# Kernel optimization log

Measured on AMD Instinct MI355X. Metric: run time of the kernel, lower is better.

Reference implementation:

```python
import jax, jax.numpy as jnp
import numpy as np

HEADS = 16
HEAD_DIM = 1024 // HEADS  # 64
SCALE = float(np.sqrt(HEAD_DIM))  # math.sqrt(features // heads)


def setup_inputs() -> dict:
    key = jax.random.key(0)
    ks = jax.random.split(key, 6)
    n, m, d, c = 2048, 2048, 1024, 768
    return {
        "x": jax.random.normal(ks[0], (n, d), dtype=jnp.float32),
        "ctx": jax.random.normal(ks[1], (m, c), dtype=jnp.float32),
        "Wq": jax.random.normal(ks[2], (d, d), dtype=jnp.float32) * (1.0 / np.sqrt(d)),
        "Wk": jax.random.normal(ks[3], (c, d), dtype=jnp.float32) * (1.0 / np.sqrt(c)),
        "Wv": jax.random.normal(ks[4], (c, d), dtype=jnp.float32) * (1.0 / np.sqrt(c)),
        "Wo": jax.random.normal(ks[5], (d, d), dtype=jnp.float32) * (1.0 / np.sqrt(d)),
    }


def reference(x, ctx, Wq, Wk, Wv, Wo):
    n, d = x.shape
    q = (x @ Wq).reshape(n, HEADS, HEAD_DIM).transpose(1, 0, 2)      # h n d
    k = (ctx @ Wk).reshape(-1, HEADS, HEAD_DIM).transpose(1, 0, 2)   # h m d
    v = (ctx @ Wv).reshape(-1, HEADS, HEAD_DIM).transpose(1, 0, 2)   # h m d
    scores = jnp.einsum("hnd,hmd->hnm", q, k) / SCALE
    attn = jax.nn.softmax(scores, axis=-1)
    out = jnp.einsum("hnm,hmd->hnd", attn, v)                        # h n d
    out = out.transpose(1, 0, 2).reshape(n, d)                       # n (h d)
    return out @ Wo
```

## Files before the change

kernel.cpp:

```cpp
#include <hip/hip_runtime.h>
#include <hip/hip_bf16.h>
#include <stdint.h>

typedef unsigned short bfu;
typedef __attribute__((ext_vector_type(8))) short short8;
typedef __attribute__((ext_vector_type(4))) float f32x4;

#define LOG2E 1.4426950408889634f

__device__ __forceinline__ bfu f2bf(float f) {
  union { float f; uint32_t u; } v; v.f = f;
  uint32_t r = (v.u + 0x7fffu + ((v.u >> 16) & 1u)) >> 16;
  return (bfu)r;
}

__device__ __forceinline__ void gload16(const void* g, void* l) {
  __builtin_amdgcn_global_load_lds((const __attribute__((address_space(1))) void*)g,
                                   (__attribute__((address_space(3))) void*)l, 16, 0, 0);
}

__device__ __forceinline__ void conv_body(const float* __restrict__ in, bfu* __restrict__ out,
                                          int i) {
  const float4* p = (const float4*)in + (size_t)i * 2;
  float4 a = p[0], b = p[1];
  union { bfu h[8]; uint4 v; } o;
  o.h[0] = f2bf(a.x); o.h[1] = f2bf(a.y); o.h[2] = f2bf(a.z); o.h[3] = f2bf(a.w);
  o.h[4] = f2bf(b.x); o.h[5] = f2bf(b.y); o.h[6] = f2bf(b.z); o.h[7] = f2bf(b.w);
  ((uint4*)out)[i] = o.v;
}

__device__ __forceinline__ void trans_body(const float* __restrict__ W, bfu* __restrict__ WT,
                                           int Kd, int n0, int k0) {
  __shared__ float tile[32][33];
  const int tx = threadIdx.x & 31, ty = threadIdx.x >> 5;
#pragma unroll
  for (int i = 0; i < 32; i += 8)
    tile[ty + i][tx] = W[(size_t)(k0 + ty + i) * 1024 + n0 + tx];
  __syncthreads();
#pragma unroll
  for (int i = 0; i < 32; i += 8)
    WT[(size_t)(n0 + ty + i) * Kd + k0 + tx] = f2bf(tile[tx][ty + i]);
}

__global__ __launch_bounds__(256) void prep_kernel(
    const float* __restrict__ x, const float* __restrict__ ctx,
    const float* __restrict__ Wq, const float* __restrict__ Wk,
    const float* __restrict__ Wv, const float* __restrict__ Wo,
    bfu* xb, bfu* ctxb, bfu* WTq, bfu* WTk, bfu* WTv, bfu* WTo) {
  int b = blockIdx.x;
  if (b < 1024)       conv_body(x, xb, b * 256 + threadIdx.x);
  else if (b < 1792)  conv_body(ctx, ctxb, (b - 1024) * 256 + threadIdx.x);
  else if (b < 2816) { b -= 1792; trans_body(Wq, WTq, 1024, (b & 31) * 32, (b >> 5) * 32); }
  else if (b < 3584) { b -= 2816; trans_body(Wk, WTk, 768, (b & 31) * 32, (b >> 5) * 32); }
  else if (b < 4352) { b -= 3584; trans_body(Wv, WTv, 768, (b & 31) * 32, (b >> 5) * 32); }
  else               { b -= 4352; trans_body(Wo, WTo, 1024, (b & 31) * 32, (b >> 5) * 32); }
}

typedef bfu Tile128[2][4][128][8];

__device__ __forceinline__ void gemm128_body(Tile128& As2, Tile128& Bs2,
    const bfu* __restrict__ A, const bfu* __restrict__ BT,
    bfu* __restrict__ Cb, int N, int K, float scale, int m0, int n0) {
  const int tid = threadIdx.x, lane = tid & 63, wave = tid >> 6;
  const int g = lane >> 4, c = lane & 15;
  const int wm = (wave >> 1) * 64, wn = (wave & 1) * 64;
  const int nt = K / 32;

  auto stage = [&](int buf, int kt) {
#pragma unroll
    for (int u = 0; u < 4; ++u) {
      int idx = wave * 4 + u;
      if (idx < 8) {
        int kg = idx & 3, rb = idx >> 2;
        gload16(&A[(size_t)(m0 + rb * 64 + lane) * K + kt + kg * 8], &As2[buf][kg][rb * 64][0]);
      } else {
        int kg = (idx - 8) & 3, rb = (idx - 8) >> 2;
        gload16(&BT[(size_t)(n0 + rb * 64 + lane) * K + kt + kg * 8], &Bs2[buf][kg][rb * 64][0]);
      }
    }
  };

  f32x4 acc[4][4] = {};
  stage(0, 0);
  for (int t = 0; t < nt; ++t) {
    __syncthreads();
    if (t + 1 < nt) stage((t + 1) & 1, (t + 1) * 32);
    const int b = t & 1;
    short8 af[4], bfr[4];
#pragma unroll
    for (int i = 0; i < 4; ++i) {
      af[i]  = *(const short8*)&As2[b][g][wm + i * 16 + c][0];
      bfr[i] = *(const short8*)&Bs2[b][g][wn + i * 16 + c][0];
    }
#pragma unroll
    for (int i = 0; i < 4; ++i)
#pragma unroll
      for (int j = 0; j < 4; ++j)
        acc[i][j] = __builtin_amdgcn_mfma_f32_16x16x32_bf16(af[i], bfr[j], acc[i][j], 0, 0, 0);
  }
#pragma unroll
  for (int i = 0; i < 4; ++i)
#pragma unroll
    for (int j = 0; j < 4; ++j) {
      int row = m0 + wm + i * 16 + g * 4;
      int col = n0 + wn + j * 16 + c;
#pragma unroll
      for (int r = 0; r < 4; ++r)
        Cb[(size_t)(row + r) * N + col] = f2bf(acc[i][j][r] * scale);
    }
}

typedef bfu AsArr[2][4][128][8];
typedef bfu BsArr[2][4][64][8];

__device__ __forceinline__ void gemm_body(AsArr& As2, BsArr& Bs2,
    const bfu* __restrict__ A, const bfu* __restrict__ BT,
    bfu* __restrict__ Cb, float* __restrict__ Cf,
    int N, int K, float scale, int m0, int n0) {
  const int tid = threadIdx.x, lane = tid & 63, wave = tid >> 6;
  const int g = lane >> 4, c = lane & 15;
  const int wm = wave * 32;
  const int nt = K / 32;

  auto stage = [&](int buf, int kt) {
#pragma unroll
    for (int u = 0; u < 3; ++u) {
      int idx = wave * 3 + u;
      if (idx < 8) {
        int g2 = idx & 3, rb = idx >> 2;
        gload16(&A[(size_t)(m0 + rb * 64 + lane) * K + kt + g2 * 8], &As2[buf][g2][rb * 64][0]);
      } else {
        int g2 = idx - 8;
        gload16(&BT[(size_t)(n0 + lane) * K + kt + g2 * 8], &Bs2[buf][g2][0][0]);
      }
    }
  };

  f32x4 acc[2][4] = {};
  stage(0, 0);
  for (int t = 0; t < nt; ++t) {
    __syncthreads();
    if (t + 1 < nt) stage((t + 1) & 1, (t + 1) * 32);
    const int b = t & 1;
    short8 af[2], bfr[4];
#pragma unroll
    for (int i = 0; i < 2; ++i) af[i] = *(const short8*)&As2[b][g][wm + i * 16 + c][0];
#pragma unroll
    for (int j = 0; j < 4; ++j) bfr[j] = *(const short8*)&Bs2[b][g][j * 16 + c][0];
#pragma unroll
    for (int i = 0; i < 2; ++i)
#pragma unroll
      for (int j = 0; j < 4; ++j)
        acc[i][j] = __builtin_amdgcn_mfma_f32_16x16x32_bf16(af[i], bfr[j], acc[i][j], 0, 0, 0);
  }
#pragma unroll
  for (int i = 0; i < 2; ++i)
#pragma unroll
    for (int j = 0; j < 4; ++j) {
      int row = m0 + wm + i * 16 + g * 4;
      int col = n0 + j * 16 + c;
#pragma unroll
      for (int r = 0; r < 4; ++r) {
        float v = acc[i][j][r] * scale;
        if (Cb) Cb[(size_t)(row + r) * N + col] = f2bf(v);
        else    Cf[(size_t)(row + r) * N + col] = v;
      }
    }
}

__global__ __launch_bounds__(256) void gemm3_kernel(
    const bfu* __restrict__ xb, const bfu* __restrict__ WTq, bfu* __restrict__ Qb,
    const bfu* __restrict__ ctxb, const bfu* __restrict__ WTk, bfu* __restrict__ Kb,
    const bfu* __restrict__ WTv, bfu* __restrict__ Vtb) {
  __shared__ alignas(16) bfu As2[2][4][128][8];
  __shared__ alignas(16) bfu Bs2[2][4][128][8];
  int bid = blockIdx.x;
  if (bid < 128)
    gemm128_body(As2, Bs2, xb, WTq, Qb, 1024, 1024, 0.125f * LOG2E, (bid >> 3) * 128, (bid & 7) * 128);
  else if (bid < 256) {
    int r = bid - 128;
    gemm128_body(As2, Bs2, ctxb, WTk, Kb, 1024, 768, 1.0f, (r >> 3) * 128, (r & 7) * 128);
  } else {
    int r = bid - 256;
    gemm_body(*(AsArr*)As2, *(BsArr*)Bs2, WTv, ctxb, Vtb, nullptr,
              2048, 768, 1.0f, (r >> 5) * 128, (r & 31) * 64);
  }
}

__global__ __launch_bounds__(256) void gemmo_kernel(const bfu* __restrict__ AO,
                                                    const bfu* __restrict__ WTo,
                                                    float* __restrict__ out) {
  __shared__ alignas(16) bfu As2[2][4][128][8];
  __shared__ alignas(16) bfu Bs2[2][4][64][8];
  int bid = blockIdx.x;
  gemm_body(As2, Bs2, AO, WTo, nullptr, out, 1024, 1024, 1.0f, (bid >> 4) * 128, (bid & 15) * 64);
}

__global__ __launch_bounds__(256) void attn_kernel(
    const bfu* __restrict__ Q, const bfu* __restrict__ Kmat,
    const bfu* __restrict__ Vt, bfu* __restrict__ O) {
  __shared__ alignas(16) bfu Ks[3][8][64][8];
  __shared__ alignas(16) bfu Vs[3][8][64][8];
  __shared__ alignas(16) bfu Ps[2][64][72];
  const int tid = threadIdx.x, wave = tid >> 6, lane = tid & 63;
  const int g = lane >> 4, c = lane & 15;
  const int bid = blockIdx.x;
  const int xcd = bid & 7, slot = bid >> 3;
  const int h = xcd + 8 * (slot >> 5);
  const int qblk = (slot & 31) * 64;
  const int col0 = h * 64;

  short8 qf[4][2];
#pragma unroll
  for (int qt = 0; qt < 4; ++qt) {
    qf[qt][0] = *(const short8*)&Q[(size_t)(qblk + qt * 16 + c) * 1024 + col0 + g * 8];
    qf[qt][1] = *(const short8*)&Q[(size_t)(qblk + qt * 16 + c) * 1024 + col0 + 32 + g * 8];
  }

  short8 ones;
#pragma unroll
  for (int e = 0; e < 8; ++e) ones[e] = (short)0x3F80;

  f32x4 o_acc[4] = {};
  f32x4 lacc = {};

  auto stage = [&](int buf, int kv0) {
#pragma unroll
    for (int u = 0; u < 4; ++u) {
      int idx = wave * 4 + u;
      if (idx < 8)
        gload16(&Kmat[(size_t)(kv0 + lane) * 1024 + col0 + idx * 8], &Ks[buf][idx][0][0]);
      else
        gload16(&Vt[(size_t)(col0 + lane) * 2048 + kv0 + (idx - 8) * 8], &Vs[buf][idx - 8][0][0]);
    }
  };

  auto qk_exp = [&](int bQ, int pb) {
    short8 kf0 = *(const short8*)&Ks[bQ][g][wave * 16 + c][0];
    short8 kf1 = *(const short8*)&Ks[bQ][4 + g][wave * 16 + c][0];
    f32x4 s[4] = {};
    __builtin_amdgcn_s_setprio(1);
#pragma unroll
    for (int qt = 0; qt < 4; ++qt) {
      s[qt] = __builtin_amdgcn_mfma_f32_16x16x32_bf16(qf[qt][0], kf0, s[qt], 0, 0, 0);
      s[qt] = __builtin_amdgcn_mfma_f32_16x16x32_bf16(qf[qt][1], kf1, s[qt], 0, 0, 0);
    }
    __builtin_amdgcn_s_setprio(0);
#pragma unroll
    for (int qt = 0; qt < 4; ++qt)
#pragma unroll
      for (int j = 0; j < 4; ++j)
        Ps[pb][qt * 16 + g * 4 + j][wave * 16 + c] =
            f2bf(__builtin_amdgcn_exp2f(s[qt][j]));
  };

  auto pv = [&](int pb, int vb) {
    __builtin_amdgcn_s_setprio(1);
#pragma unroll
    for (int kc = 0; kc < 2; ++kc) {
      short8 pf = *(const short8*)&Ps[pb][wave * 16 + c][kc * 32 + g * 8];
      lacc = __builtin_amdgcn_mfma_f32_16x16x32_bf16(pf, ones, lacc, 0, 0, 0);
#pragma unroll
      for (int fd = 0; fd < 4; ++fd) {
        short8 vf = *(const short8*)&Vs[vb][kc * 4 + g][fd * 16 + c][0];
        o_acc[fd] = __builtin_amdgcn_mfma_f32_16x16x32_bf16(pf, vf, o_acc[fd], 0, 0, 0);
      }
    }
    __builtin_amdgcn_s_setprio(0);
  };

  stage(0, 0);
  __syncthreads();
  stage(1, 64);
  qk_exp(0, 0);
  __syncthreads();
  for (int t = 1; t < 32; ++t) {
    stage((t + 1) % 3, ((t + 1) & 31) * 64);
    qk_exp(t % 3, t & 1);
    pv((t - 1) & 1, (t - 1) % 3);
    __syncthreads();
  }
  pv(1, 1);

  const int q0 = qblk + wave * 16;
#pragma unroll
  for (int fd = 0; fd < 4; ++fd)
#pragma unroll
    for (int j = 0; j < 4; ++j) {
      float v = o_acc[fd][j] / lacc[j];
      O[(size_t)(q0 + g * 4 + j) * 1024 + col0 + fd * 16 + c] = f2bf(v);
    }
}

extern "C" void kernel_launch(void* const* d_in, const int* in_sizes, int n_in,
                              void* d_out, int out_size, void* d_ws, size_t ws_size,
                              hipStream_t stream) {
  const float* x   = (const float*)d_in[0];
  const float* ctx = (const float*)d_in[1];
  const float* Wq  = (const float*)d_in[2];
  const float* Wk  = (const float*)d_in[3];
  const float* Wv  = (const float*)d_in[4];
  const float* Wo  = (const float*)d_in[5];
  float* out = (float*)d_out;

  bfu* ws   = (bfu*)d_ws;
  bfu* xb   = ws;
  bfu* WTk  = xb + 2048 * 1024;
  bfu* WTv  = WTk + 1024 * 768;
  bfu* WTo  = WTv + 1024 * 768;
  bfu* Qb   = WTo + 1024 * 1024;
  bfu* Kb   = Qb + 2048 * 1024;
  bfu* Vtb  = Kb + 2048 * 1024;
  bfu* WTq  = (bfu*)d_out;
  bfu* ctxb = WTq + 1024 * 1024;

  dim3 blk(256);
  prep_kernel<<<5376, blk, 0, stream>>>(x, ctx, Wq, Wk, Wv, Wo, xb, ctxb, WTq, WTk, WTv, WTo);
  gemm3_kernel<<<512, blk, 0, stream>>>(xb, WTq, Qb, ctxb, WTk, Kb, WTv, Vtb);
  attn_kernel<<<512, blk, 0, stream>>>(Qb, Kb, Vtb, xb);
  gemmo_kernel<<<256, blk, 0, stream>>>(xb, WTo, out);
}
```

Before: 106.8 us.

## Rewrite output projection GEMM with 64x64 tiles, 128-thread blocks, XCD-aware mapping

The output projection GEMM gets a dedicated kernel that uses 64x64 output tiles and 128-thread blocks, launching 512 blocks instead of 256. Each block's tile is chosen from an XCD-aware mapping of the block id. The goal is more blocks to fill the GPU's compute units, and better L2 locality on the 2048x1024 by 1024x1024 GEMM. The cost is less reuse per block, a different K-tile schedule, and scalar stores of the fp32 output that may coalesce poorly.

```diff
diff --git a/kernel.cpp b/kernel.cpp
--- a/kernel.cpp
+++ b/kernel.cpp
@@ -187,13 +187,60 @@
   }
 }
 
-__global__ __launch_bounds__(256) void gemmo_kernel(const bfu* __restrict__ AO,
+typedef bfu T64[2][4][64][8];
+
+__global__ __launch_bounds__(128) void gemmo_kernel(const bfu* __restrict__ AO,
                                                     const bfu* __restrict__ WTo,
                                                     float* __restrict__ out) {
-  __shared__ alignas(16) bfu As2[2][4][128][8];
+  __shared__ alignas(16) bfu As2[2][4][64][8];
   __shared__ alignas(16) bfu Bs2[2][4][64][8];
-  int bid = blockIdx.x;
-  gemm_body(As2, Bs2, AO, WTo, nullptr, out, 1024, 1024, 1.0f, (bid >> 4) * 128, (bid & 15) * 64);
+  const int tid = threadIdx.x, lane = tid & 63, wave = tid >> 6;
+  const int g = lane >> 4, c = lane & 15;
+  const int bid = blockIdx.x;
+  const int xcd = bid & 7, slot = bid >> 3;
+  const int m0 = (xcd * 4 + (slot >> 4)) * 64;
+  const int n0 = (slot & 15) * 64;
+  const int wm = wave * 32;
+  const int K = 1024, N = 1024, nt = 32;
+
+  auto stage = [&](int buf, int kt) {
+#pragma unroll
+    for (int u = 0; u < 4; ++u) {
+      int idx = wave * 4 + u;
+      if (idx < 4)
+        gload16(&AO[(size_t)(m0 + lane) * K + kt + idx * 8], &As2[buf][idx][lane][0]);
+      else
+        gload16(&WTo[(size_t)(n0 + lane) * K + kt + (idx - 4) * 8], &Bs2[buf][idx - 4][lane][0]);
+    }
+  };
+
+  f32x4 acc[2][4] = {};
+  stage(0, 0);
+  for (int t = 0; t < nt; ++t) {
+    __syncthreads();
+    if (t + 1 < nt) stage((t + 1) & 1, (t + 1) * 32);
+    const int b = t & 1;
+    short8 af[2], bfr[4];
+#pragma unroll
+    for (int i = 0; i < 2; ++i) af[i] = *(const short8*)&As2[b][g][wm + i * 16 + c][0];
+#pragma unroll
+    for (int j = 0; j < 4; ++j) bfr[j] = *(const short8*)&Bs2[b][g][j * 16 + c][0];
+#pragma unroll
+    for (int i = 0; i < 2; ++i)
+#pragma unroll
+      for (int j = 0; j < 4; ++j)
+        acc[i][j] = __builtin_amdgcn_mfma_f32_16x16x32_bf16(af[i], bfr[j], acc[i][j], 0, 0, 0);
+  }
+#pragma unroll
+  for (int i = 0; i < 2; ++i)
+#pragma unroll
+    for (int j = 0; j < 4; ++j) {
+      int row = m0 + wm + i * 16 + g * 4;
+      int col = n0 + j * 16 + c;
+#pragma unroll
+      for (int r = 0; r < 4; ++r)
+        out[(size_t)(row + r) * N + col] = acc[i][j][r];
+    }
 }
 
 __global__ __launch_bounds__(256) void attn_kernel(
@@ -318,5 +365,5 @@
   prep_kernel<<<5376, blk, 0, stream>>>(x, ctx, Wq, Wk, Wv, Wo, xb, ctxb, WTq, WTk, WTv, WTo);
   gemm3_kernel<<<512, blk, 0, stream>>>(xb, WTq, Qb, ctxb, WTk, Kb, WTv, Vtb);
   attn_kernel<<<512, blk, 0, stream>>>(Qb, Kb, Vtb, xb);
-  gemmo_kernel<<<256, blk, 0, stream>>>(xb, WTo, out);
-}
+  gemmo_kernel<<<512, dim3(128), 0, stream>>>(xb, WTo, out);
+}
```

Result: no change. 106.1 us (-0.7%).
